# Optimization experiments

Measured on AMD Instinct MI355X. Metric: run time of the kernel, lower is better.

Reference implementation:

```python
import jax, jax.numpy as jnp
import numpy as np

N = 8192
C = 256


def setup_inputs() -> dict:
    key = jax.random.key(0)
    k_x, k_wr, k_br, k_wc, k_bc = jax.random.split(key, 5)
    scale = 1.0 / np.sqrt(C)
    return {
        "x": jax.random.normal(k_x, (N, C), dtype=jnp.float32),
        "w_reduce": jax.random.uniform(k_wr, (C, C), dtype=jnp.float32, minval=-scale, maxval=scale),
        "b_reduce": jax.random.uniform(k_br, (C,), dtype=jnp.float32, minval=-scale, maxval=scale),
        "w_contr": jax.random.uniform(k_wc, (1, C), dtype=jnp.float32, minval=-scale, maxval=scale),
        "b_contr": jax.random.uniform(k_bc, (1,), dtype=jnp.float32, minval=-scale, maxval=scale),
    }


def reference(x, w_reduce, b_reduce, w_contr, b_contr):
    # Original math: y_ij = reduce(x_i + x_j); z_ij = sigmoid(contr(y_ij));
    # out_i = mean_j y_ij * z_ij.
    # Since reduce/contr are affine, decompose without the [N,N,C] tensor:
    #   y_ij = r_i + r_j + b_reduce,        r = x @ Wr^T
    #   contr(y_ij) = s_i + s_j + c0,       s = r . wc, c0 = b_reduce . wc + bc
    n = x.shape[0]
    r = x @ w_reduce.T                                   # [N, C]
    wc = w_contr[0]                                      # [C]
    s = r @ wc                                           # [N]
    c0 = b_reduce @ wc + b_contr[0]                      # scalar
    Z = jax.nn.sigmoid(s[:, None] + s[None, :] + c0)     # [N, N] pairwise gate
    m = jnp.mean(Z, axis=1, keepdims=True)               # [N, 1]
    # mean_j (r_i + r_j + b) * z_ij = (r_i + b) * m_i + (Z @ r)_i / N
    out = (r + b_reduce) * m + (Z @ r) / n               # [N, C]
    return out
```

## Files before the change

kernel.cpp:

```cpp
#include <hip/hip_runtime.h>
#include <hip/hip_bf16.h>
#include <stdint.h>

#define NN 8192
#define CC 256
#define NSPLIT 8
#define JR (NN / NSPLIT)
#define NITER (JR / 32)

typedef float f32x4 __attribute__((ext_vector_type(4)));
typedef float f32x2 __attribute__((ext_vector_type(2)));
typedef short s16x8 __attribute__((ext_vector_type(8)));

#define LOG2E 1.4426950408889634f

#define OFF_WT  0
#define OFF_R   (OFF_WT + CC*CC)
#define OFF_S2  (OFF_R + NN*CC)
#define OFF_C0  (OFF_S2 + NN)
#define OFF_SS  (OFF_C0 + 16)
#define OFF_SP  (OFF_SS + NSPLIT*NN)
#define OFF_V   (OFF_SP + 4*NN)
#define OFF_RB  (OFF_V + (NSPLIT*NN*CC)/2)

__global__ __launch_bounds__(256) void k_prep(const float* __restrict__ w,
                                              const float* __restrict__ br,
                                              const float* __restrict__ wcv,
                                              const float* __restrict__ bc,
                                              float* __restrict__ ws) {
  int k = blockIdx.x, c = threadIdx.x;
  ws[OFF_WT + k * CC + c] = w[c * CC + k];
  if (blockIdx.x == 0 && threadIdx.x < 64) {
    int lane = threadIdx.x;
    f32x4 b4 = *(const f32x4*)&br[lane * 4];
    f32x4 w4 = *(const f32x4*)&wcv[lane * 4];
    float d = b4[0]*w4[0] + b4[1]*w4[1] + b4[2]*w4[2] + b4[3]*w4[3];
    #pragma unroll
    for (int m = 32; m >= 1; m >>= 1) d += __shfl_xor(d, m, 64);
    if (lane == 0) { ws[OFF_C0] = d + bc[0]; ws[OFF_C0 + 1] = (d + bc[0]) * LOG2E; }
  }
}

__global__ __launch_bounds__(256) void k_r(const float* __restrict__ x,
                                           const float* __restrict__ wcv,
                                           float* __restrict__ ws) {
  __shared__ float xs[64][260];
  int bi = blockIdx.x;
  int rowblk = bi >> 2, colblk = bi & 3;
  int tid = threadIdx.x;
  int i0 = rowblk * 64;
  for (int t = tid; t < 64 * 64; t += 256) {
    int rr = t >> 6, c4 = t & 63;
    *(f32x4*)&xs[rr][c4 * 4] = *(const f32x4*)&x[(i0 + rr) * CC + c4 * 4];
  }
  __syncthreads();
  int tx = tid & 15, ty = tid >> 4;
  int cbase = colblk * 64 + tx * 4;
  int r0 = ty * 4;
  float acc[4][4] = {};
  const float* wt = ws + OFF_WT;
  for (int k = 0; k < CC; k += 2) {
    f32x4 wv0 = *(const f32x4*)&wt[k * CC + cbase];
    f32x4 wv1 = *(const f32x4*)&wt[(k + 1) * CC + cbase];
    f32x2 xv[4];
    #pragma unroll
    for (int rr = 0; rr < 4; rr++) xv[rr] = *(const f32x2*)&xs[r0 + rr][k];
    #pragma unroll
    for (int rr = 0; rr < 4; rr++)
      #pragma unroll
      for (int cc = 0; cc < 4; cc++)
        acc[rr][cc] = fmaf(xv[rr][1], wv1[cc], fmaf(xv[rr][0], wv0[cc], acc[rr][cc]));
  }
  #pragma unroll
  for (int rr = 0; rr < 4; rr++) {
    f32x4 o = {acc[rr][0], acc[rr][1], acc[rr][2], acc[rr][3]};
    *(f32x4*)&ws[OFF_R + (size_t)(i0 + r0 + rr) * CC + cbase] = o;
  }
  unsigned long long* rb64 = (unsigned long long*)(ws + OFF_RB);
  int j0r = i0 + r0;
  #pragma unroll
  for (int cc = 0; cc < 4; cc++) {
    int c = cbase + cc;
    unsigned long long v = 0;
    #pragma unroll
    for (int rr = 0; rr < 4; rr++) {
      unsigned u = __float_as_uint(acc[rr][cc]);
      u = (u + 0x7fffu + ((u >> 16) & 1u)) >> 16;
      v |= (unsigned long long)u << (16 * rr);
    }
    int us = (((j0r >> 5) * 16 + (c >> 4)) * 64 + (((j0r >> 3) & 3) * 16 + (c & 15))) * 8 + (j0r & 7);
    rb64[us >> 2] = v;
  }
  f32x4 wc4 = *(const f32x4*)&wcv[cbase];
  float sd[4];
  #pragma unroll
  for (int rr = 0; rr < 4; rr++) {
    sd[rr] = acc[rr][0]*wc4[0] + acc[rr][1]*wc4[1] + acc[rr][2]*wc4[2] + acc[rr][3]*wc4[3];
    #pragma unroll
    for (int m = 1; m < 16; m <<= 1) sd[rr] += __shfl_xor(sd[rr], m, 64);
  }
  if (tx == 0) {
    #pragma unroll
    for (int rr = 0; rr < 4; rr++)
      ws[OFF_SP + colblk * NN + j0r + rr] = sd[rr];
  }
}

__global__ __launch_bounds__(256) void k_s2(float* __restrict__ ws) {
  int row = blockIdx.x * 256 + threadIdx.x;
  float s = ws[OFF_SP + row] + ws[OFF_SP + NN + row]
          + ws[OFF_SP + 2 * NN + row] + ws[OFF_SP + 3 * NN + row];
  ws[OFF_S2 + row] = s * LOG2E;
}


#define STAGE(BUF, IT) { \
  const char* gb_ = rbase + (size_t)(IT) * 16384 + w * 1024 + l * 16; \
  _Pragma("unroll") \
  for (int q_ = 0; q_ < 4; q_++) \
    __builtin_amdgcn_global_load_lds( \
      (const __attribute__((address_space(1))) void*)(gb_ + q_ * 4096), \
      (__attribute__((address_space(3))) void*)&ldsb[(BUF) * 16384 + w * 1024 + q_ * 4096], \
      16, 0, 0); }

#define WAITBAR4 { asm volatile("s_waitcnt vmcnt(4)" ::: "memory"); \
  __builtin_amdgcn_s_barrier(); \
  __builtin_amdgcn_sched_barrier(0); }

#define WAITBAR0 { asm volatile("s_waitcnt vmcnt(0)" ::: "memory"); \
  __builtin_amdgcn_s_barrier(); \
  __builtin_amdgcn_sched_barrier(0); }

#define SB0 __builtin_amdgcn_sched_barrier(0);

#define SIGMOID(IT, AFA, AFB) { \
  f32x4 sj0_ = *(const f32x4*)&s2l[(IT) * 32 + g * 8]; \
  f32x4 sj1_ = *(const f32x4*)&s2l[(IT) * 32 + g * 8 + 4]; \
  _Pragma("unroll") \
  for (int t_ = 0; t_ < 8; t_++) { \
    float sj_ = (t_ < 4) ? sj0_[t_] : sj1_[t_ - 4]; \
    float eA_, eB_; \
    asm("v_exp_f32 %0, %1" : "=v"(eA_) : "v"(negaA - sj_)); \
    asm("v_exp_f32 %0, %1" : "=v"(eB_) : "v"(negaB - sj_)); \
    float zA_ = __builtin_amdgcn_rcpf(1.0f + eA_); \
    float zB_ = __builtin_amdgcn_rcpf(1.0f + eB_); \
    (AFA)[t_] = (short)(__float_as_uint(zA_) >> 16); \
    (AFB)[t_] = (short)(__float_as_uint(zB_) >> 16); } }

#define MFMA_PHASE(AFA, AFB, LP) { \
  _Pragma("unroll") \
  for (int ct_ = 0; ct_ < 16; ct_++) { \
    s16x8 bf_ = *(const s16x8*)((LP) + ct_ * 1024 + l * 16); \
    accA[ct_] = __builtin_amdgcn_mfma_f32_16x16x32_bf16(AFA, bf_, accA[ct_], 0, 0, 0); \
    accB[ct_] = __builtin_amdgcn_mfma_f32_16x16x32_bf16(AFB, bf_, accB[ct_], 0, 0, 0); } \
  acc1A = __builtin_amdgcn_mfma_f32_16x16x32_bf16(AFA, ones, acc1A, 0, 0, 0); \
  acc1B = __builtin_amdgcn_mfma_f32_16x16x32_bf16(AFB, ones, acc1B, 0, 0, 0); }

__global__ __launch_bounds__(256, 2) void k_main(float* __restrict__ ws) {
  __shared__ char ldsb[3 * 16384];
  __shared__ float s2l[1024];
  int blk = blockIdx.x;
  int rt = blk >> 3, h = blk & 7;
  int tid = threadIdx.x;
  int w = tid >> 6, l = tid & 63;
  int lr = l & 15, g = l >> 4;
  int iw = rt * 128 + w * 32;
  float c02 = ws[OFF_C0 + 1];
  float negaA = -(ws[OFF_S2 + iw + lr] + c02);
  float negaB = -(ws[OFF_S2 + iw + 16 + lr] + c02);

  const float* s2p = ws + OFF_S2 + h * JR;
  *(f32x4*)&s2l[tid * 4] = *(const f32x4*)(s2p + tid * 4);
  __syncthreads();

  f32x4 accA[16], accB[16], acc1A, acc1B;
  #pragma unroll
  for (int i = 0; i < 16; i++) { accA[i] = (f32x4)(0.f); accB[i] = (f32x4)(0.f); }
  acc1A = (f32x4)(0.f); acc1B = (f32x4)(0.f);
  s16x8 ones;
  #pragma unroll
  for (int t = 0; t < 8; t++) ones[t] = (short)0x3F80;

  const char* rbase = (const char*)(ws + OFF_RB) + (size_t)h * (JR * CC * 2);

  STAGE(0, 0);
  STAGE(1, 1);
  s16x8 afA0, afB0, afA1, afB1;
  SIGMOID(0, afA0, afB0);

  int sA = 0;
  #pragma unroll 1
  for (int J = 0; J < NITER - 2; J += 2) {
    int sB = sA + 1; if (sB == 3) sB = 0;
    int sC = sB + 1; if (sC == 3) sC = 0;

    WAITBAR4;
    STAGE(sC, J + 2);
    SB0;
    SIGMOID(J + 1, afA1, afB1);
    MFMA_PHASE(afA0, afB0, ldsb + sA * 16384);

    WAITBAR4;
    STAGE(sA, J + 3);
    SB0;
    SIGMOID(J + 2, afA0, afB0);
    MFMA_PHASE(afA1, afB1, ldsb + sB * 16384);

    sA = sC;
  }
  {
    int sB = sA + 1; if (sB == 3) sB = 0;
    WAITBAR4;
    SIGMOID(NITER - 1, afA1, afB1);
    MFMA_PHASE(afA0, afB0, ldsb + sA * 16384);
    WAITBAR0;
    MFMA_PHASE(afA1, afB1, ldsb + sB * 16384);
  }

  if (lr == 0) {
    #pragma unroll
    for (int q = 0; q < 4; q++) {
      ws[OFF_SS + h * NN + iw + g * 4 + q] = acc1A[q];
      ws[OFF_SS + h * NN + iw + 16 + g * 4 + q] = acc1B[q];
    }
  }
  unsigned short* Vb = (unsigned short*)(ws + OFF_V);
  size_t vbase = (size_t)h * (NN * CC);
  #pragma unroll
  for (int ct = 0; ct < 16; ct++) {
    #pragma unroll
    for (int q = 0; q < 4; q++) {
      unsigned uA = __float_as_uint(accA[ct][q]);
      uA = (uA + 0x7fffu + ((uA >> 16) & 1u)) >> 16;
      Vb[vbase + (size_t)(iw + g * 4 + q) * CC + ct * 16 + lr] = (unsigned short)uA;
      unsigned uB = __float_as_uint(accB[ct][q]);
      uB = (uB + 0x7fffu + ((uB >> 16) & 1u)) >> 16;
      Vb[vbase + (size_t)(iw + 16 + g * 4 + q) * CC + ct * 16 + lr] = (unsigned short)uB;
    }
  }
}

__global__ __launch_bounds__(256) void k_epi(const float* __restrict__ br,
                                             const float* __restrict__ ws,
                                             float* __restrict__ out) {
  int idx = blockIdx.x * 256 + threadIdx.x;
  int i = idx >> 5, c8 = (idx & 31) * 8;
  float S = 0.f;
  #pragma unroll
  for (int p = 0; p < NSPLIT; p++) S += ws[OFF_SS + p * NN + i];
  float m = S * (1.0f / NN);
  float v[8] = {};
  const unsigned short* Vb = (const unsigned short*)(ws + OFF_V);
  #pragma unroll
  for (int p = 0; p < NSPLIT; p++) {
    s16x8 pv = *(const s16x8*)&Vb[(size_t)p * (NN * CC) + (size_t)i * CC + c8];
    #pragma unroll
    for (int t = 0; t < 8; t++)
      v[t] += __uint_as_float(((unsigned)(unsigned short)pv[t]) << 16);
  }
  f32x4 r0 = *(const f32x4*)&ws[OFF_R + (size_t)i * CC + c8];
  f32x4 r1 = *(const f32x4*)&ws[OFF_R + (size_t)i * CC + c8 + 4];
  f32x4 b0 = *(const f32x4*)&br[c8];
  f32x4 b1 = *(const f32x4*)&br[c8 + 4];
  f32x4 o0, o1;
  #pragma unroll
  for (int t = 0; t < 4; t++) {
    o0[t] = (r0[t] + b0[t]) * m + v[t] * (1.0f / NN);
    o1[t] = (r1[t] + b1[t]) * m + v[t + 4] * (1.0f / NN);
  }
  *(f32x4*)&out[(size_t)i * CC + c8] = o0;
  *(f32x4*)&out[(size_t)i * CC + c8 + 4] = o1;
}

extern "C" void kernel_launch(void* const* d_in, const int* in_sizes, int n_in,
                              void* d_out, int out_size, void* d_ws, size_t ws_size,
                              hipStream_t stream) {
  const float* x  = (const float*)d_in[0];
  const float* w  = (const float*)d_in[1];
  const float* br = (const float*)d_in[2];
  const float* wc = (const float*)d_in[3];
  const float* bc = (const float*)d_in[4];
  float* ws = (float*)d_ws;
  float* out = (float*)d_out;
  (void)in_sizes; (void)n_in; (void)out_size; (void)ws_size;

  k_prep<<<256, 256, 0, stream>>>(w, br, wc, bc, ws);
  k_r<<<512, 256, 0, stream>>>(x, wc, ws);
  k_s2<<<32, 256, 0, stream>>>(ws);
  k_main<<<512, 256, 0, stream>>>(ws);
  k_epi<<<1024, 256, 0, stream>>>(br, ws, out);
}
```

Measured before the change: 83.79 us.

## Shrink main kernel blocks to two waves with a simple double buffer

The main pairwise-gate GEMM kernel now runs 128-thread blocks covering 64 rows each, launched as 1024 blocks instead of 512. The triple-buffered, two-stage software pipeline, which computed the next sigmoid ahead and waited with a partial vmcnt, is replaced by a plain double-buffered loop that waits for all loads and barriers every iteration. Each wave now issues 8 async global-to-LDS copies per stage instead of 4. The aim is more resident blocks and less LDS per block, at the cost of losing load/compute overlap and taking a full memory wait each iteration. Each block also re-reads the same r tiles for fewer rows, which doubles global traffic for the operand.

```diff
diff --git a/kernel.cpp b/kernel.cpp
--- a/kernel.cpp
+++ b/kernel.cpp
@@ -117,15 +117,11 @@
 #define STAGE(BUF, IT) { \
   const char* gb_ = rbase + (size_t)(IT) * 16384 + w * 1024 + l * 16; \
   _Pragma("unroll") \
-  for (int q_ = 0; q_ < 4; q_++) \
+  for (int q_ = 0; q_ < 8; q_++) \
     __builtin_amdgcn_global_load_lds( \
-      (const __attribute__((address_space(1))) void*)(gb_ + q_ * 4096), \
-      (__attribute__((address_space(3))) void*)&ldsb[(BUF) * 16384 + w * 1024 + q_ * 4096], \
+      (const __attribute__((address_space(1))) void*)(gb_ + q_ * 2048), \
+      (__attribute__((address_space(3))) void*)&ldsb[(BUF) * 16384 + w * 1024 + q_ * 2048 + l * 16], \
       16, 0, 0); }
-
-#define WAITBAR4 { asm volatile("s_waitcnt vmcnt(4)" ::: "memory"); \
-  __builtin_amdgcn_s_barrier(); \
-  __builtin_amdgcn_sched_barrier(0); }
 
 #define WAITBAR0 { asm volatile("s_waitcnt vmcnt(0)" ::: "memory"); \
   __builtin_amdgcn_s_barrier(); \
@@ -156,21 +152,22 @@
   acc1A = __builtin_amdgcn_mfma_f32_16x16x32_bf16(AFA, ones, acc1A, 0, 0, 0); \
   acc1B = __builtin_amdgcn_mfma_f32_16x16x32_bf16(AFB, ones, acc1B, 0, 0, 0); }
 
-__global__ __launch_bounds__(256, 2) void k_main(float* __restrict__ ws) {
-  __shared__ char ldsb[3 * 16384];
+__global__ __launch_bounds__(128, 2) void k_main(float* __restrict__ ws) {
+  __shared__ char ldsb[2 * 16384];
   __shared__ float s2l[1024];
   int blk = blockIdx.x;
   int rt = blk >> 3, h = blk & 7;
   int tid = threadIdx.x;
   int w = tid >> 6, l = tid & 63;
   int lr = l & 15, g = l >> 4;
-  int iw = rt * 128 + w * 32;
+  int iw = rt * 64 + w * 32;
   float c02 = ws[OFF_C0 + 1];
   float negaA = -(ws[OFF_S2 + iw + lr] + c02);
   float negaB = -(ws[OFF_S2 + iw + 16 + lr] + c02);
 
   const float* s2p = ws + OFF_S2 + h * JR;
   *(f32x4*)&s2l[tid * 4] = *(const f32x4*)(s2p + tid * 4);
+  *(f32x4*)&s2l[(tid + 128) * 4] = *(const f32x4*)(s2p + (tid + 128) * 4);
   __syncthreads();
 
   f32x4 accA[16], accB[16], acc1A, acc1B;
@@ -184,37 +181,14 @@
   const char* rbase = (const char*)(ws + OFF_RB) + (size_t)h * (JR * CC * 2);
 
   STAGE(0, 0);
-  STAGE(1, 1);
-  s16x8 afA0, afB0, afA1, afB1;
-  SIGMOID(0, afA0, afB0);
-
-  int sA = 0;
+  s16x8 afA, afB;
   #pragma unroll 1
-  for (int J = 0; J < NITER - 2; J += 2) {
-    int sB = sA + 1; if (sB == 3) sB = 0;
-    int sC = sB + 1; if (sC == 3) sC = 0;
-
-    WAITBAR4;
-    STAGE(sC, J + 2);
+  for (int J = 0; J < NITER; ++J) {
+    WAITBAR0;
+    if (J + 1 < NITER) STAGE((J + 1) & 1, J + 1);
     SB0;
-    SIGMOID(J + 1, afA1, afB1);
-    MFMA_PHASE(afA0, afB0, ldsb + sA * 16384);
-
-    WAITBAR4;
-    STAGE(sA, J + 3);
-    SB0;
-    SIGMOID(J + 2, afA0, afB0);
-    MFMA_PHASE(afA1, afB1, ldsb + sB * 16384);
-
-    sA = sC;
-  }
-  {
-    int sB = sA + 1; if (sB == 3) sB = 0;
-    WAITBAR4;
-    SIGMOID(NITER - 1, afA1, afB1);
-    MFMA_PHASE(afA0, afB0, ldsb + sA * 16384);
-    WAITBAR0;
-    MFMA_PHASE(afA1, afB1, ldsb + sB * 16384);
+    SIGMOID(J, afA, afB);
+    MFMA_PHASE(afA, afB, ldsb + (J & 1) * 16384);
   }
 
   if (lr == 0) {
@@ -287,6 +261,6 @@
   k_prep<<<256, 256, 0, stream>>>(w, br, wc, bc, ws);
   k_r<<<512, 256, 0, stream>>>(x, wc, ws);
   k_s2<<<32, 256, 0, stream>>>(ws);
-  k_main<<<512, 256, 0, stream>>>(ws);
+  k_main<<<1024, 128, 0, stream>>>(ws);
   k_epi<<<1024, 256, 0, stream>>>(br, ws, out);
 }
```

Measured after the change: 85.01 us. Within noise of the previous version (+1.5%).
